# Kernel tuning notes

Measured on AMD Instinct MI355X. Metric: run time of the kernel, lower is better.

The kernel has to match this reference:

```python
import jax, jax.numpy as jnp
import numpy as np

D_MODEL = 1024
NUM_HEADS = 16
GROUPS = 4
HEADS_PER_GROUP = NUM_HEADS // GROUPS
D_K = D_MODEL // NUM_HEADS
B, S = 2, 2048


def setup_inputs() -> dict:
    key = jax.random.key(0)
    ks = jax.random.split(key, 10)
    sc = 0.02
    return {
        "x": jax.random.normal(ks[0], (B, S, D_MODEL), dtype=jnp.float32),
        "W_Q": jax.random.normal(ks[1], (D_MODEL, D_MODEL), dtype=jnp.float32) * sc,
        "b_Q": jnp.zeros((D_MODEL,), dtype=jnp.float32),
        "W_K": jax.random.normal(ks[2], (GROUPS, D_MODEL, D_K), dtype=jnp.float32) * sc,
        "b_K": jnp.zeros((GROUPS, D_K), dtype=jnp.float32),
        "W_V": jax.random.normal(ks[3], (GROUPS, D_MODEL, D_K), dtype=jnp.float32) * sc,
        "b_V": jnp.zeros((GROUPS, D_K), dtype=jnp.float32),
        "W_O": jax.random.normal(ks[4], (D_MODEL, D_MODEL), dtype=jnp.float32) * sc,
        "b_O": jnp.zeros((D_MODEL,), dtype=jnp.float32),
    }


def reference(x, W_Q, b_Q, W_K, b_K, W_V, b_V, W_O, b_O):
    b, s, _ = x.shape
    # Q: [b, s, d_model] -> [b, groups, heads_per_group, s, d_k]
    Q = (x @ W_Q + b_Q).reshape(b, s, NUM_HEADS, D_K).transpose(0, 2, 1, 3)
    Q = Q.reshape(b, GROUPS, HEADS_PER_GROUP, s, D_K)
    # Shared K/V per group: [b, groups, s, d_k]
    K = jnp.einsum('bsd,gdk->bgsk', x, W_K) + b_K[None, :, None, :]
    V = jnp.einsum('bsd,gdk->bgsk', x, W_V) + b_V[None, :, None, :]
    # scores: [b, groups, heads_per_group, s, s]
    scores = jnp.einsum('bghsk,bgtk->bghst', Q, K) / jnp.sqrt(jnp.float32(D_K))
    attn = jax.nn.softmax(scores, axis=-1)
    # context: [b, groups, heads_per_group, s, d_k] -> [b, s, d_model]
    ctx = jnp.einsum('bghst,bgtk->bghsk', attn, V)
    ctx = ctx.reshape(b, NUM_HEADS, s, D_K).transpose(0, 2, 1, 3).reshape(b, s, D_MODEL)
    return ctx @ W_O + b_O
```

## Files before the change

### kernel.cpp

```cpp
#include <hip/hip_runtime.h>
#include <cstdint>
#include <cstddef>

typedef short bf16x8 __attribute__((ext_vector_type(8)));
typedef float f32x4 __attribute__((ext_vector_type(4)));

#define DM 1024
#define NHEADS 16
#define NGROUPS 4
#define DK 64
#define BATCH 2
#define SEQ 2048
#define MROWS 4096

#define QB_ELEMS   ((size_t)BATCH*NHEADS*SEQ*DK)
#define KB_ELEMS   ((size_t)BATCH*NGROUPS*SEQ*DK)
#define VT_ELEMS   KB_ELEMS
#define XC_ELEMS   ((size_t)MROWS*DM)
#define WQKV_ELEMS ((size_t)1536*DM)
#define WO_ELEMS   ((size_t)DM*DM)

__device__ __forceinline__ ushort f2bf(float f) {
    union { float f; uint32_t u; } a; a.f = f;
    uint32_t u = a.u;
    return (ushort)((u + 0x7FFFu + ((u >> 16) & 1u)) >> 16);
}
__device__ __forceinline__ ushort f2bf_rh(float f) {
    union { float f; uint32_t u; } a; a.f = f;
    return (ushort)((a.u + 0x8000u) >> 16);
}

__device__ __forceinline__ void gll16(const void* g, void* l) {
    __builtin_amdgcn_global_load_lds((const __attribute__((address_space(1))) void*)g,
                                     (__attribute__((address_space(3))) void*)l, 16, 0, 0);
}

__global__ __launch_bounds__(256) void gqa_prep_kernel(
        const float* __restrict__ x,
        const float* __restrict__ WQ, const float* __restrict__ WK,
        const float* __restrict__ WV, const float* __restrict__ WO,
        const float* __restrict__ bQ, const float* __restrict__ bK,
        const float* __restrict__ bV,
        ushort* __restrict__ xbf, ushort* __restrict__ WqkvT,
        ushort* __restrict__ WoT, float* __restrict__ bcat)
{
    __shared__ float tl[64][65];
    const int bid = blockIdx.x, tid = threadIdx.x;
    if (bid < 640) {
        const float* src; ushort* dst; int src_ld; int r0, c0;
        if (bid < 256) {
            src = WQ; src_ld = 1024; dst = WqkvT;
            r0 = (bid >> 4) * 64; c0 = (bid & 15) * 64;
        } else if (bid < 512) {
            int t = bid - 256;
            src = WO; src_ld = 1024; dst = WoT;
            r0 = (t >> 4) * 64; c0 = (t & 15) * 64;
        } else if (bid < 576) {
            int t = bid - 512; int g = t >> 4;
            src = WK + (size_t)g * 1024 * 64; src_ld = 64;
            dst = WqkvT + (size_t)(1024 + g * 64) * 1024;
            r0 = (t & 15) * 64; c0 = 0;
        } else {
            int t = bid - 576; int g = t >> 4;
            src = WV + (size_t)g * 1024 * 64; src_ld = 64;
            dst = WqkvT + (size_t)(1280 + g * 64) * 1024;
            r0 = (t & 15) * 64; c0 = 0;
        }
        const int rr = tid >> 4, cc = (tid & 15) * 4;
#pragma unroll
        for (int p = 0; p < 4; p++) {
            int r = rr + p * 16;
            float4 v = *(const float4*)(src + (size_t)(r0 + r) * src_ld + c0 + cc);
            tl[cc + 0][r] = v.x; tl[cc + 1][r] = v.y;
            tl[cc + 2][r] = v.z; tl[cc + 3][r] = v.w;
        }
        __syncthreads();
#pragma unroll
        for (int p = 0; p < 4; p++) {
            int c = rr + p * 16;
            ushort4 o;
            o.x = f2bf(tl[c][cc + 0]); o.y = f2bf(tl[c][cc + 1]);
            o.z = f2bf(tl[c][cc + 2]); o.w = f2bf(tl[c][cc + 3]);
            *(ushort4*)(dst + (size_t)(c0 + c) * 1024 + r0 + cc) = o;
        }
    } else if (bid < 896) {
        int cid = bid - 640;
        const float* xs = x + (size_t)cid * 16384;
        ushort* xd = xbf + (size_t)cid * 16384;
#pragma unroll
        for (int p = 0; p < 16; p++) {
            float4 v = *(const float4*)(xs + p * 1024 + tid * 4);
            ushort4 o = { f2bf(v.x), f2bf(v.y), f2bf(v.z), f2bf(v.w) };
            *(ushort4*)(xd + p * 1024 + tid * 4) = o;
        }
    } else {
        for (int i = tid; i < 1536; i += 256) {
            float v = (i < 1024) ? bQ[i] : (i < 1280 ? bK[i - 1024] : bV[i - 1280]);
            bcat[i] = v;
        }
    }
}

template<bool QKV_EPI>
__global__ __launch_bounds__(256, 2) void gqa_gemm_kernel(
        const ushort* __restrict__ A, const ushort* __restrict__ BT,
        const float* __restrict__ bias, float* __restrict__ outF,
        ushort* __restrict__ Qb, ushort* __restrict__ Kb, ushort* __restrict__ Vtg)
{
    __shared__ ushort As[2][128 * 64];
    __shared__ ushort Bs[2][128 * 64];
    const int tid = threadIdx.x;
    const int bm = blockIdx.x, bn = blockIdx.y;
    const int wave = tid >> 6, lane = tid & 63;
    const int wm = (wave & 1) * 64, wn = (wave >> 1) * 64;
    const int lr = lane & 15, lq = lane >> 4;
    const int swz = lr & 7;

    const int cb = (lane & 7) ^ (lane >> 3);
    const ushort* srcA[4]; const ushort* srcB[4]; int dstOff[4];
#pragma unroll
    for (int seg = 0; seg < 4; seg++) {
        int row = seg * 32 + wave * 8 + (lane >> 3);
        srcA[seg] = A  + (size_t)(bm * 128 + row) * 1024 + cb * 8;
        srcB[seg] = BT + (size_t)(bn * 128 + row) * 1024 + cb * 8;
        dstOff[seg] = seg * 2048 + wave * 512;
    }

    f32x4 acc[4][4];
#pragma unroll
    for (int i = 0; i < 4; i++)
#pragma unroll
        for (int j = 0; j < 4; j++) acc[i][j] = (f32x4){0.f, 0.f, 0.f, 0.f};

#pragma unroll
    for (int seg = 0; seg < 4; seg++) {
        gll16(srcA[seg], &As[0][dstOff[seg]]);
        gll16(srcB[seg], &Bs[0][dstOff[seg]]);
    }

    for (int kt = 0; kt < 16; kt++) {
        __syncthreads();
        if (kt < 15) {
            int buf = (kt + 1) & 1, ko = (kt + 1) * 64;
#pragma unroll
            for (int seg = 0; seg < 4; seg++) {
                gll16(srcA[seg] + ko, &As[buf][dstOff[seg]]);
                gll16(srcB[seg] + ko, &Bs[buf][dstOff[seg]]);
            }
        }
        const ushort* as = As[kt & 1];
        const ushort* bs = Bs[kt & 1];
        bf16x8 af[2][4], bfr[2][4];
#pragma unroll
        for (int kh = 0; kh < 2; kh++) {
#pragma unroll
            for (int i = 0; i < 4; i++)
                af[kh][i] = *(const bf16x8*)&as[(wm + i * 16 + lr) * 64 + (((kh * 4 + lq) ^ swz)) * 8];
#pragma unroll
            for (int j = 0; j < 4; j++)
                bfr[kh][j] = *(const bf16x8*)&bs[(wn + j * 16 + lr) * 64 + (((kh * 4 + lq) ^ swz)) * 8];
        }
#pragma unroll
        for (int kh = 0; kh < 2; kh++)
#pragma unroll
            for (int i = 0; i < 4; i++)
#pragma unroll
                for (int j = 0; j < 4; j++)
                    acc[i][j] = __builtin_amdgcn_mfma_f32_16x16x32_bf16(af[kh][i], bfr[kh][j], acc[i][j], 0, 0, 0);
    }

#pragma unroll
    for (int i = 0; i < 4; i++) {
        int mg = bm * 128 + wm + i * 16 + lq * 4;
        int b = mg >> 11, s = mg & 2047;
#pragma unroll
        for (int j = 0; j < 4; j++) {
            int cg = bn * 128 + wn + j * 16 + lr;
            float bv = bias[cg];
            if constexpr (QKV_EPI) {
                int d = cg & 63;
                if (cg < 1024) {
                    int h = cg >> 6;
                    ushort* dst = Qb + ((size_t)(b * NHEADS + h) * SEQ + s) * DK + d;
#pragma unroll
                    for (int r = 0; r < 4; r++) dst[r * DK] = f2bf(acc[i][j][r] + bv);
                } else if (cg < 1280) {
                    int g = (cg - 1024) >> 6;
                    ushort* dst = Kb + ((size_t)(b * NGROUPS + g) * SEQ + s) * DK + d;
#pragma unroll
                    for (int r = 0; r < 4; r++) dst[r * DK] = f2bf(acc[i][j][r] + bv);
                } else {
                    int g = (cg - 1280) >> 6;
                    int s4 = s >> 2, kg = s4 & 7;
                    int col = ((s4 >> 3) << 5) + (((((kg & 3) << 1) | (kg >> 2))) << 2);
                    ushort4 pk;
                    pk.x = f2bf(acc[i][j][0] + bv); pk.y = f2bf(acc[i][j][1] + bv);
                    pk.z = f2bf(acc[i][j][2] + bv); pk.w = f2bf(acc[i][j][3] + bv);
                    *(ushort4*)(Vtg + ((size_t)(b * NGROUPS + g) * DK + d) * SEQ + col) = pk;
                }
            } else {
#pragma unroll
                for (int r = 0; r < 4; r++)
                    outF[(size_t)(mg + r) * DM + cg] = acc[i][j][r] + bv;
            }
        }
    }
}

__global__ __launch_bounds__(128, 2) void gqa_attn_kernel(
        const ushort* __restrict__ Qb, const ushort* __restrict__ Kb,
        const ushort* __restrict__ Vtg, ushort* __restrict__ ctx)
{
    __shared__ ushort Ks[2][64 * 64];
    __shared__ ushort Vs[2][64 * 64];

    const int tid = threadIdx.x, wave = tid >> 6, lane = tid & 63;
    const int lr = lane & 15, lq = lane >> 4;
    const int swz = lr & 7;
    const int blk = blockIdx.x;
    const int qt = blk & 31, bh = blk >> 5;
    const int b = bh >> 4, hg = bh & 15, g = hg >> 2;

    const ushort* Qh = Qb  + (size_t)(b * NHEADS  + hg) * SEQ * DK;
    const ushort* Kg = Kb  + (size_t)(b * NGROUPS + g)  * SEQ * DK;
    const ushort* Vg = Vtg + (size_t)(b * NGROUPS + g)  * DK * SEQ;

    const int s0 = qt * 64 + wave * 32;

    bf16x8 qf[2][2];
#pragma unroll
    for (int qs = 0; qs < 2; qs++)
#pragma unroll
        for (int h = 0; h < 2; h++)
            qf[qs][h] = *(const bf16x8*)(Qh + (size_t)(s0 + qs * 16 + lr) * DK + h * 32 + lq * 8);

    const int cb = (lane & 7) ^ (lane >> 3);
    const ushort* srcK[4]; const ushort* srcV[4]; int dstOff[4];
#pragma unroll
    for (int seg = 0; seg < 4; seg++) {
        int row = wave * 32 + seg * 8 + (lane >> 3);
        srcK[seg] = Kg + (size_t)row * DK + cb * 8;
        srcV[seg] = Vg + (size_t)row * SEQ + cb * 8;
        dstOff[seg] = wave * 2048 + seg * 512;
    }

    f32x4 of[2][4];
#pragma unroll
    for (int qs = 0; qs < 2; qs++)
#pragma unroll
        for (int j = 0; j < 4; j++) of[qs][j] = (f32x4){0.f, 0.f, 0.f, 0.f};
    float lsum[2] = {0.f, 0.f};

    const float SCL = 0.125f * 1.44269504f;

#pragma unroll
    for (int seg = 0; seg < 4; seg++) {
        gll16(srcK[seg], &Ks[0][dstOff[seg]]);
        gll16(srcV[seg], &Vs[0][dstOff[seg]]);
    }

    for (int it = 0; it < 32; it++) {
        __syncthreads();
        if (it < 31) {
            int buf = (it + 1) & 1, t0 = (it + 1) * 64;
#pragma unroll
            for (int seg = 0; seg < 4; seg++) {
                gll16(srcK[seg] + (size_t)t0 * DK, &Ks[buf][dstOff[seg]]);
                gll16(srcV[seg] + t0, &Vs[buf][dstOff[seg]]);
            }
        }
        const ushort* ks = Ks[it & 1];
        const ushort* vs = Vs[it & 1];

        bf16x8 kf[4][2];
#pragma unroll
        for (int nt = 0; nt < 4; nt++)
#pragma unroll
            for (int h = 0; h < 2; h++)
                kf[nt][h] = *(const bf16x8*)&ks[((nt * 16 + lr) * 8 + ((h * 4 + lq) ^ swz)) * 8];

        f32x4 sc[2][4];
#pragma unroll
        for (int qs = 0; qs < 2; qs++)
#pragma unroll
            for (int nt = 0; nt < 4; nt++) {
                f32x4 s = (f32x4){0.f, 0.f, 0.f, 0.f};
                s = __builtin_amdgcn_mfma_f32_16x16x32_bf16(kf[nt][0], qf[qs][0], s, 0, 0, 0);
                s = __builtin_amdgcn_mfma_f32_16x16x32_bf16(kf[nt][1], qf[qs][1], s, 0, 0, 0);
                sc[qs][nt] = s;
            }

        union { bf16x8 v; ushort u[8]; } pf[2][2];
#pragma unroll
        for (int qs = 0; qs < 2; qs++)
#pragma unroll
            for (int nt = 0; nt < 4; nt++)
#pragma unroll
                for (int r = 0; r < 4; r++) {
                    float p = __builtin_amdgcn_exp2f(sc[qs][nt][r] * SCL);
                    lsum[qs] += p;
                    pf[qs][nt >> 1].u[(nt & 1) * 4 + r] = f2bf_rh(p);
                }

        bf16x8 vf[4][2];
#pragma unroll
        for (int j = 0; j < 4; j++)
#pragma unroll
            for (int kh = 0; kh < 2; kh++)
                vf[j][kh] = *(const bf16x8*)&vs[((j * 16 + lr) * 8 + ((kh * 4 + lq) ^ swz)) * 8];

#pragma unroll
        for (int qs = 0; qs < 2; qs++)
#pragma unroll
            for (int j = 0; j < 4; j++) {
                of[qs][j] = __builtin_amdgcn_mfma_f32_16x16x32_bf16(vf[j][0], pf[qs][0].v, of[qs][j], 0, 0, 0);
                of[qs][j] = __builtin_amdgcn_mfma_f32_16x16x32_bf16(vf[j][1], pf[qs][1].v, of[qs][j], 0, 0, 0);
            }
    }

    float inv[2];
#pragma unroll
    for (int qs = 0; qs < 2; qs++) {
        float v = lsum[qs];
        v += __shfl_xor(v, 16);
        v += __shfl_xor(v, 32);
        inv[qs] = 1.0f / v;
    }
    ushort* cbp = ctx + (size_t)b * SEQ * DM;
#pragma unroll
    for (int qs = 0; qs < 2; qs++) {
        int s = s0 + qs * 16 + lr;
#pragma unroll
        for (int j = 0; j < 4; j++) {
            ushort4 o;
            o.x = f2bf(of[qs][j][0] * inv[qs]);
            o.y = f2bf(of[qs][j][1] * inv[qs]);
            o.z = f2bf(of[qs][j][2] * inv[qs]);
            o.w = f2bf(of[qs][j][3] * inv[qs]);
            *(ushort4*)(cbp + (size_t)s * DM + hg * 64 + j * 16 + lq * 4) = o;
        }
    }
}

extern "C" void kernel_launch(void* const* d_in, const int* in_sizes, int n_in,
                              void* d_out, int out_size, void* d_ws, size_t ws_size,
                              hipStream_t stream) {
    const float* x  = (const float*)d_in[0];
    const float* WQ = (const float*)d_in[1];
    const float* bQ = (const float*)d_in[2];
    const float* WK = (const float*)d_in[3];
    const float* bK = (const float*)d_in[4];
    const float* WV = (const float*)d_in[5];
    const float* bV = (const float*)d_in[6];
    const float* WO = (const float*)d_in[7];
    const float* bO = (const float*)d_in[8];

    ushort* Qb    = (ushort*)d_ws;
    ushort* Kb    = Qb + QB_ELEMS;
    ushort* Vtg   = Kb + KB_ELEMS;
    ushort* xc    = Vtg + VT_ELEMS;
    ushort* WqkvT = xc + XC_ELEMS;
    ushort* WoT   = WqkvT + WQKV_ELEMS;
    float*  bcat  = (float*)(WoT + WO_ELEMS);

    gqa_prep_kernel<<<897, 256, 0, stream>>>(x, WQ, WK, WV, WO, bQ, bK, bV,
                                             xc, WqkvT, WoT, bcat);
    gqa_gemm_kernel<true><<<dim3(32, 12), 256, 0, stream>>>(
        xc, WqkvT, bcat, nullptr, Qb, Kb, Vtg);
    gqa_attn_kernel<<<1024, 128, 0, stream>>>(Qb, Kb, Vtg, xc);
    gqa_gemm_kernel<false><<<dim3(32, 8), 256, 0, stream>>>(
        xc, WoT, bO, (float*)d_out, nullptr, nullptr, nullptr);
}
```

Measured before the change: 185.1 us.

## Retile GEMMs to 128x64, enlarge attention blocks, compute row sums via MFMA

The GEMM tile shrinks from 128x128 to 128x64, doubling the grid so more blocks cover the CUs. The attention kernel moves to 256 threads covering 128 query rows, so each K/V tile loaded into LDS is shared by twice as many waves. The softmax scale and log2e are folded into Q in the QKV epilogue. Row sums are computed with an MFMA against a ones vector, and bf16 packing uses a truncating perm instead of rounding. The smaller GEMM tiles reduce data reuse per block, and the truncated P values and the absence of max subtraction are accuracy risks.

```diff
diff --git a/kernel.cpp b/kernel.cpp
--- a/kernel.cpp
+++ b/kernel.cpp
@@ -20,14 +20,12 @@
 #define WQKV_ELEMS ((size_t)1536*DM)
 #define WO_ELEMS   ((size_t)DM*DM)
 
+#define SCL_Q 0.180336880f
+
 __device__ __forceinline__ ushort f2bf(float f) {
     union { float f; uint32_t u; } a; a.f = f;
     uint32_t u = a.u;
     return (ushort)((u + 0x7FFFu + ((u >> 16) & 1u)) >> 16);
-}
-__device__ __forceinline__ ushort f2bf_rh(float f) {
-    union { float f; uint32_t u; } a; a.f = f;
-    return (ushort)((a.u + 0x8000u) >> 16);
 }
 
 __device__ __forceinline__ void gll16(const void* g, void* l) {
@@ -108,64 +106,69 @@
         ushort* __restrict__ Qb, ushort* __restrict__ Kb, ushort* __restrict__ Vtg)
 {
     __shared__ ushort As[2][128 * 64];
-    __shared__ ushort Bs[2][128 * 64];
+    __shared__ ushort Bs[2][64 * 64];
     const int tid = threadIdx.x;
     const int bm = blockIdx.x, bn = blockIdx.y;
     const int wave = tid >> 6, lane = tid & 63;
-    const int wm = (wave & 1) * 64, wn = (wave >> 1) * 64;
+    const int wm = (wave & 1) * 64, wn = (wave >> 1) * 32;
     const int lr = lane & 15, lq = lane >> 4;
     const int swz = lr & 7;
 
-    const int cb = (lane & 7) ^ (lane >> 3);
-    const ushort* srcA[4]; const ushort* srcB[4]; int dstOff[4];
-#pragma unroll
-    for (int seg = 0; seg < 4; seg++) {
-        int row = seg * 32 + wave * 8 + (lane >> 3);
-        srcA[seg] = A  + (size_t)(bm * 128 + row) * 1024 + cb * 8;
-        srcB[seg] = BT + (size_t)(bn * 128 + row) * 1024 + cb * 8;
-        dstOff[seg] = seg * 2048 + wave * 512;
-    }
-
-    f32x4 acc[4][4];
+    const ushort* srcA[4]; int dstA[4];
+    const ushort* srcB[2]; int dstB[2];
+#pragma unroll
+    for (int p = 0; p < 4; p++) {
+        int slot = p * 256 + tid;
+        int row = slot >> 3, cb = (slot & 7) ^ (row & 7);
+        srcA[p] = A + (size_t)(bm * 128 + row) * 1024 + cb * 8;
+        dstA[p] = p * 2048 + wave * 512;
+    }
+#pragma unroll
+    for (int p = 0; p < 2; p++) {
+        int slot = p * 256 + tid;
+        int row = slot >> 3, cb = (slot & 7) ^ (row & 7);
+        srcB[p] = BT + (size_t)(bn * 64 + row) * 1024 + cb * 8;
+        dstB[p] = p * 2048 + wave * 512;
+    }
+
+    f32x4 acc[4][2];
 #pragma unroll
     for (int i = 0; i < 4; i++)
 #pragma unroll
-        for (int j = 0; j < 4; j++) acc[i][j] = (f32x4){0.f, 0.f, 0.f, 0.f};
-
-#pragma unroll
-    for (int seg = 0; seg < 4; seg++) {
-        gll16(srcA[seg], &As[0][dstOff[seg]]);
-        gll16(srcB[seg], &Bs[0][dstOff[seg]]);
-    }
+        for (int j = 0; j < 2; j++) acc[i][j] = (f32x4){0.f, 0.f, 0.f, 0.f};
+
+#pragma unroll
+    for (int p = 0; p < 4; p++) gll16(srcA[p], &As[0][dstA[p]]);
+#pragma unroll
+    for (int p = 0; p < 2; p++) gll16(srcB[p], &Bs[0][dstB[p]]);
 
     for (int kt = 0; kt < 16; kt++) {
         __syncthreads();
         if (kt < 15) {
             int buf = (kt + 1) & 1, ko = (kt + 1) * 64;
 #pragma unroll
-            for (int seg = 0; seg < 4; seg++) {
-                gll16(srcA[seg] + ko, &As[buf][dstOff[seg]]);
-                gll16(srcB[seg] + ko, &Bs[buf][dstOff[seg]]);
-            }
+            for (int p = 0; p < 4; p++) gll16(srcA[p] + ko, &As[buf][dstA[p]]);
+#pragma unroll
+            for (int p = 0; p < 2; p++) gll16(srcB[p] + ko, &Bs[buf][dstB[p]]);
         }
         const ushort* as = As[kt & 1];
         const ushort* bs = Bs[kt & 1];
-        bf16x8 af[2][4], bfr[2][4];
+        bf16x8 af[2][4], bfr[2][2];
 #pragma unroll
         for (int kh = 0; kh < 2; kh++) {
 #pragma unroll
             for (int i = 0; i < 4; i++)
-                af[kh][i] = *(const bf16x8*)&as[(wm + i * 16 + lr) * 64 + (((kh * 4 + lq) ^ swz)) * 8];
-#pragma unroll
-            for (int j = 0; j < 4; j++)
-                bfr[kh][j] = *(const bf16x8*)&bs[(wn + j * 16 + lr) * 64 + (((kh * 4 + lq) ^ swz)) * 8];
+                af[kh][i] = *(const bf16x8*)&as[(wm + i * 16 + lr) * 64 + ((kh * 4 + lq) ^ swz) * 8];
+#pragma unroll
+            for (int j = 0; j < 2; j++)
+                bfr[kh][j] = *(const bf16x8*)&bs[(wn + j * 16 + lr) * 64 + ((kh * 4 + lq) ^ swz) * 8];
         }
 #pragma unroll
         for (int kh = 0; kh < 2; kh++)
 #pragma unroll
             for (int i = 0; i < 4; i++)
 #pragma unroll
-                for (int j = 0; j < 4; j++)
+                for (int j = 0; j < 2; j++)
                     acc[i][j] = __builtin_amdgcn_mfma_f32_16x16x32_bf16(af[kh][i], bfr[kh][j], acc[i][j], 0, 0, 0);
     }
 
@@ -174,8 +177,8 @@
         int mg = bm * 128 + wm + i * 16 + lq * 4;
         int b = mg >> 11, s = mg & 2047;
 #pragma unroll
-        for (int j = 0; j < 4; j++) {
-            int cg = bn * 128 + wn + j * 16 + lr;
+        for (int j = 0; j < 2; j++) {
+            int cg = bn * 64 + wn + j * 16 + lr;
             float bv = bias[cg];
             if constexpr (QKV_EPI) {
                 int d = cg & 63;
@@ -183,7 +186,8 @@
                     int h = cg >> 6;
                     ushort* dst = Qb + ((size_t)(b * NHEADS + h) * SEQ + s) * DK + d;
 #pragma unroll
-                    for (int r = 0; r < 4; r++) dst[r * DK] = f2bf(acc[i][j][r] + bv);
+                    for (int r = 0; r < 4; r++)
+                        dst[r * DK] = f2bf((acc[i][j][r] + bv) * SCL_Q);
                 } else if (cg < 1280) {
                     int g = (cg - 1024) >> 6;
                     ushort* dst = Kb + ((size_t)(b * NGROUPS + g) * SEQ + s) * DK + d;
@@ -207,7 +211,7 @@
     }
 }
 
-__global__ __launch_bounds__(128, 2) void gqa_attn_kernel(
+__global__ __launch_bounds__(256, 2) void gqa_attn_kernel(
         const ushort* __restrict__ Qb, const ushort* __restrict__ Kb,
         const ushort* __restrict__ Vtg, ushort* __restrict__ ctx)
 {
@@ -218,14 +222,14 @@
     const int lr = lane & 15, lq = lane >> 4;
     const int swz = lr & 7;
     const int blk = blockIdx.x;
-    const int qt = blk & 31, bh = blk >> 5;
+    const int qt = blk & 15, bh = blk >> 4;
     const int b = bh >> 4, hg = bh & 15, g = hg >> 2;
 
     const ushort* Qh = Qb  + (size_t)(b * NHEADS  + hg) * SEQ * DK;
     const ushort* Kg = Kb  + (size_t)(b * NGROUPS + g)  * SEQ * DK;
     const ushort* Vg = Vtg + (size_t)(b * NGROUPS + g)  * DK * SEQ;
 
-    const int s0 = qt * 64 + wave * 32;
+    const int s0 = qt * 128 + wave * 32;
 
     bf16x8 qf[2][2];
 #pragma unroll
@@ -234,14 +238,14 @@
         for (int h = 0; h < 2; h++)
             qf[qs][h] = *(const bf16x8*)(Qh + (size_t)(s0 + qs * 16 + lr) * DK + h * 32 + lq * 8);
 
-    const int cb = (lane & 7) ^ (lane >> 3);
-    const ushort* srcK[4]; const ushort* srcV[4]; int dstOff[4];
-#pragma unroll
-    for (int seg = 0; seg < 4; seg++) {
-        int row = wave * 32 + seg * 8 + (lane >> 3);
-        srcK[seg] = Kg + (size_t)row * DK + cb * 8;
-        srcV[seg] = Vg + (size_t)row * SEQ + cb * 8;
-        dstOff[seg] = wave * 2048 + seg * 512;
+    const ushort* srcK[2]; const ushort* srcV[2]; int dstOff[2];
+#pragma unroll
+    for (int p = 0; p < 2; p++) {
+        int slot = p * 256 + tid;
+        int row = slot >> 3, cb = (slot & 7) ^ (row & 7);
+        srcK[p] = Kg + (size_t)row * DK + cb * 8;
+        srcV[p] = Vg + (size_t)row * SEQ + cb * 8;
+        dstOff[p] = p * 2048 + wave * 512;
     }
 
     f32x4 of[2][4];
@@ -249,14 +253,16 @@
     for (int qs = 0; qs < 2; qs++)
 #pragma unroll
         for (int j = 0; j < 4; j++) of[qs][j] = (f32x4){0.f, 0.f, 0.f, 0.f};
-    float lsum[2] = {0.f, 0.f};
-
-    const float SCL = 0.125f * 1.44269504f;
-
-#pragma unroll
-    for (int seg = 0; seg < 4; seg++) {
-        gll16(srcK[seg], &Ks[0][dstOff[seg]]);
-        gll16(srcV[seg], &Vs[0][dstOff[seg]]);
+    f32x4 accL[2] = {(f32x4){0.f,0.f,0.f,0.f}, (f32x4){0.f,0.f,0.f,0.f}};
+
+    bf16x8 ones;
+#pragma unroll
+    for (int i = 0; i < 8; i++) ones[i] = (short)0x3F80;
+
+#pragma unroll
+    for (int p = 0; p < 2; p++) {
+        gll16(srcK[p], &Ks[0][dstOff[p]]);
+        gll16(srcV[p], &Vs[0][dstOff[p]]);
     }
 
     for (int it = 0; it < 32; it++) {
@@ -264,9 +270,9 @@
         if (it < 31) {
             int buf = (it + 1) & 1, t0 = (it + 1) * 64;
 #pragma unroll
-            for (int seg = 0; seg < 4; seg++) {
-                gll16(srcK[seg] + (size_t)t0 * DK, &Ks[buf][dstOff[seg]]);
-                gll16(srcV[seg] + t0, &Vs[buf][dstOff[seg]]);
+            for (int p = 0; p < 2; p++) {
+                gll16(srcK[p] + (size_t)t0 * DK, &Ks[buf][dstOff[p]]);
+                gll16(srcV[p] + t0, &Vs[buf][dstOff[p]]);
             }
         }
         const ushort* ks = Ks[it & 1];
@@ -290,17 +296,23 @@
                 sc[qs][nt] = s;
             }
 
-        union { bf16x8 v; ushort u[8]; } pf[2][2];
-#pragma unroll
-        for (int qs = 0; qs < 2; qs++)
-#pragma unroll
-            for (int nt = 0; nt < 4; nt++)
-#pragma unroll
-                for (int r = 0; r < 4; r++) {
-                    float p = __builtin_amdgcn_exp2f(sc[qs][nt][r] * SCL);
-                    lsum[qs] += p;
-                    pf[qs][nt >> 1].u[(nt & 1) * 4 + r] = f2bf_rh(p);
-                }
+        union PF { bf16x8 v; uint32_t w[4]; };
+        PF pf[2][2];
+#pragma unroll
+        for (int qs = 0; qs < 2; qs++) {
+#pragma unroll
+            for (int nt = 0; nt < 4; nt++) {
+                union { float f; uint32_t u; } e0, e1, e2, e3;
+                e0.f = __builtin_amdgcn_exp2f(sc[qs][nt][0]);
+                e1.f = __builtin_amdgcn_exp2f(sc[qs][nt][1]);
+                e2.f = __builtin_amdgcn_exp2f(sc[qs][nt][2]);
+                e3.f = __builtin_amdgcn_exp2f(sc[qs][nt][3]);
+                pf[qs][nt >> 1].w[(nt & 1) * 2 + 0] = __builtin_amdgcn_perm(e1.u, e0.u, 0x07060302u);
+                pf[qs][nt >> 1].w[(nt & 1) * 2 + 1] = __builtin_amdgcn_perm(e3.u, e2.u, 0x07060302u);
+            }
+            accL[qs] = __builtin_amdgcn_mfma_f32_16x16x32_bf16(ones, pf[qs][0].v, accL[qs], 0, 0, 0);
+            accL[qs] = __builtin_amdgcn_mfma_f32_16x16x32_bf16(ones, pf[qs][1].v, accL[qs], 0, 0, 0);
+        }
 
         bf16x8 vf[4][2];
 #pragma unroll
@@ -319,13 +331,9 @@
     }
 
     float inv[2];
-#pragma unroll
-    for (int qs = 0; qs < 2; qs++) {
-        float v = lsum[qs];
-        v += __shfl_xor(v, 16);
-        v += __shfl_xor(v, 32);
-        inv[qs] = 1.0f / v;
-    }
+    inv[0] = 1.0f / accL[0][0];
+    inv[1] = 1.0f / accL[1][0];
+
     ushort* cbp = ctx + (size_t)b * SEQ * DM;
 #pragma unroll
     for (int qs = 0; qs < 2; qs++) {
@@ -365,9 +373,9 @@
 
     gqa_prep_kernel<<<897, 256, 0, stream>>>(x, WQ, WK, WV, WO, bQ, bK, bV,
                                              xc, WqkvT, WoT, bcat);
-    gqa_gemm_kernel<true><<<dim3(32, 12), 256, 0, stream>>>(
+    gqa_gemm_kernel<true><<<dim3(32, 24), 256, 0, stream>>>(
         xc, WqkvT, bcat, nullptr, Qb, Kb, Vtg);
-    gqa_attn_kernel<<<1024, 128, 0, stream>>>(Qb, Kb, Vtg, xc);
-    gqa_gemm_kernel<false><<<dim3(32, 8), 256, 0, stream>>>(
+    gqa_attn_kernel<<<512, 256, 0, stream>>>(Qb, Kb, Vtg, xc);
+    gqa_gemm_kernel<false><<<dim3(32, 16), 256, 0, stream>>>(
         xc, WoT, bO, (float*)d_out, nullptr, nullptr, nullptr);
 }
```

New measurement: 162.9 us. -12.0%, faster.
